# Optimization experiments

Measured on AMD Instinct MI355X. Metric: run time of the kernel, lower is better.

Reference implementation:

```python
import math
import jax, jax.numpy as jnp
import numpy as np

N_HEADS = 16
NUM_BUCKETS = 32
MAX_DISTANCE = 128
ROTARY_BASE = 10000.0


def rotate_half(x):
    x1, x2 = jnp.split(x, 2, axis=-1)
    return jnp.concatenate((-x2, x1), axis=-1)


def rotary_freqs(T, dim):
    inv_freq = 1.0 / (ROTARY_BASE ** (jnp.arange(0, dim, 2, dtype=jnp.float32) / dim))
    t = jnp.arange(T, dtype=jnp.float32)
    freqs = jnp.einsum('i,j->ij', t, inv_freq)  # [T, dim/2]
    return jnp.concatenate((freqs, freqs), axis=-1)  # [T, dim]


def rel_pos_bucket_causal(rel_pos, num_buckets=NUM_BUCKETS, max_distance=MAX_DISTANCE):
    n = jnp.maximum(-rel_pos, 0)  # [T, T] int
    max_exact = num_buckets // 2
    is_small = n < max_exact
    n_safe = jnp.maximum(n, 1).astype(jnp.float32)
    val_if_large = max_exact + (
        jnp.log(n_safe / max_exact) / math.log(max_distance / max_exact) * (num_buckets - max_exact)
    ).astype(jnp.int32)
    val_if_large = jnp.minimum(val_if_large, num_buckets - 1)
    return jnp.where(is_small, n, val_if_large)


def setup_inputs() -> dict:
    key = jax.random.key(0)
    ks = jax.random.split(key, 10)
    B, T, C = 2, 2048, 1024
    s = 0.02
    return {
        'x':  jax.random.normal(ks[0], (B, T, C), dtype=jnp.float32),
        'Wq': jax.random.normal(ks[1], (C, C), dtype=jnp.float32) * s,
        'bq': jnp.zeros((C,), dtype=jnp.float32),
        'Wk': jax.random.normal(ks[2], (C, C), dtype=jnp.float32) * s,
        'bk': jnp.zeros((C,), dtype=jnp.float32),
        'Wv': jax.random.normal(ks[3], (C, C), dtype=jnp.float32) * s,
        'bv': jnp.zeros((C,), dtype=jnp.float32),
        'Wp': jax.random.normal(ks[4], (C, C), dtype=jnp.float32) * s,
        'bp': jnp.zeros((C,), dtype=jnp.float32),
        'rel_bias_table': jax.random.normal(ks[5], (NUM_BUCKETS, N_HEADS), dtype=jnp.float32) * s,
    }


def reference(x, Wq, bq, Wk, bk, Wv, bv, Wp, bp, rel_bias_table):
    B, T, C = x.shape
    H = N_HEADS
    D = C // H

    def heads(y):
        return y.reshape(B, T, H, D).transpose(0, 2, 1, 3)  # [B,H,T,D]

    q = heads(x @ Wq + bq)
    k = heads(x @ Wk + bk)
    v = heads(x @ Wv + bv)

    # rotary (use_xpos=False -> scale=1)
    freqs = rotary_freqs(T, D)  # [T, D]
    cos, sin = jnp.cos(freqs), jnp.sin(freqs)
    q = q * cos + rotate_half(q) * sin
    k = k * cos + rotate_half(k) * sin

    # relative position bias (causal, scale=1.0)
    pos = jnp.arange(T)
    rel_pos = pos[None, :] - pos[:, None]  # k_pos - q_pos
    bucket = rel_pos_bucket_causal(rel_pos)  # [T, T]
    bias = rel_bias_table[bucket]  # [T, T, H]
    bias = bias.transpose(2, 0, 1)  # [H, T, T]

    att = jnp.einsum('bhid,bhjd->bhij', q, k) + bias[None]
    att = att * (1.0 / math.sqrt(D))
    causal = pos[None, :] <= pos[:, None]  # tril mask [T, T]
    att = jnp.where(causal[None, None], att, -jnp.inf)
    att = jax.nn.softmax(att, axis=-1)

    y = jnp.einsum('bhij,bhjd->bhid', att, v)  # [B,H,T,D]
    y = y.transpose(0, 2, 1, 3).reshape(B, T, C)
    return y @ Wp + bp
```

## Files before the change

kernel.cpp:

```cpp
#include <hip/hip_runtime.h>
#include <hip/hip_bf16.h>
#include <math.h>

#define B_ 2
#define T_ 2048
#define C_ 1024
#define H_ 16
#define D_ 64
#define M_ (B_ * T_)
#define K_ 1024

#define SCALE2 0.18033688011112043f

typedef short bf16x8 __attribute__((ext_vector_type(8)));
typedef float f32x4  __attribute__((ext_vector_type(4)));
typedef unsigned int u32;

__device__ __forceinline__ float u2f(unsigned short u) {
    union { unsigned int i; float f; } v; v.i = ((unsigned int)u) << 16; return v.f;
}
__device__ __forceinline__ unsigned short f2b(float f) {
    __hip_bfloat16 h = __float2bfloat16(f);
    return *reinterpret_cast<unsigned short*>(&h);
}
__device__ __forceinline__ u32 pack_bf16_rnd(float a, float b) {
    const u32 au = __float_as_uint(a) + 0x8000u;
    const u32 bu = __float_as_uint(b) + 0x8000u;
    return __builtin_amdgcn_perm(bu, au, 0x07060302u);
}
__device__ __forceinline__ void load_lds16(const void* g, void* l) {
    __builtin_amdgcn_global_load_lds(
        (const __attribute__((address_space(1))) u32*)g,
        (__attribute__((address_space(3))) u32*)l, 16, 0, 0);
}

__global__ __launch_bounds__(256) void prep(
    const float* __restrict__ x,
    const float* __restrict__ W0, const float* __restrict__ W1,
    const float* __restrict__ W2, const float* __restrict__ W3,
    const float* __restrict__ tbl,
    unsigned short* __restrict__ xb,
    unsigned short* __restrict__ T0, unsigned short* __restrict__ T1,
    unsigned short* __restrict__ T2, unsigned short* __restrict__ T3,
    float* __restrict__ dtab, float2* __restrict__ trig)
{
    __shared__ __align__(16) unsigned short tile[64][72];
    const int bx = blockIdx.x;
    const int tid = threadIdx.x;

    if (bx < 2048) {
        const int idx = bx * 256 + tid;
        const float4 a = reinterpret_cast<const float4*>(x)[idx * 2];
        const float4 b = reinterpret_cast<const float4*>(x)[idx * 2 + 1];
        unsigned short t[8] = {f2b(a.x), f2b(a.y), f2b(a.z), f2b(a.w),
                               f2b(b.x), f2b(b.y), f2b(b.z), f2b(b.w)};
        reinterpret_cast<bf16x8*>(xb)[idx] = *reinterpret_cast<const bf16x8*>(t);
    } else if (bx < 3072) {
        const int w = bx - 2048;
        const int z = w >> 8;
        const int rem = w & 255;
        const int k0 = (rem & 15) * 64, n0 = (rem >> 4) * 64;
        const float* W = z == 0 ? W0 : z == 1 ? W1 : z == 2 ? W2 : W3;
        unsigned short* Wt = z == 0 ? T0 : z == 1 ? T1 : z == 2 ? T2 : T3;

        #pragma unroll
        for (int it = 0; it < 4; ++it) {
            const int idx = it * 256 + tid;
            const int r = idx >> 4, c = (idx & 15) * 4;
            const float4 w4 = *reinterpret_cast<const float4*>(W + (size_t)(k0 + r) * C_ + n0 + c);
            tile[r][c + 0] = f2b(w4.x); tile[r][c + 1] = f2b(w4.y);
            tile[r][c + 2] = f2b(w4.z); tile[r][c + 3] = f2b(w4.w);
        }
        __syncthreads();
        #pragma unroll
        for (int it = 0; it < 2; ++it) {
            const int idx = it * 256 + tid;
            const int nc = idx >> 3, kc = (idx & 7) * 8;
            unsigned short tmp[8];
            #pragma unroll
            for (int e = 0; e < 8; ++e) tmp[e] = tile[kc + e][nc];
            *reinterpret_cast<bf16x8*>(Wt + (size_t)(n0 + nc) * K_ + k0 + kc) =
                *reinterpret_cast<const bf16x8*>(tmp);
        }
    } else {
        const int idx = (bx - 3072) * 256 + tid;
        if (idx < H_ * T_) {
            const int h = idx >> 11, n = idx & (T_ - 1);
            int bucket;
            if (n < 16) bucket = n;
            else {
                int vb = 16 + (int)(log2f((float)n * 0.0625f) * (16.0f / 3.0f));
                bucket = vb < 31 ? vb : 31;
            }
            dtab[idx] = tbl[bucket * H_ + h] * SCALE2;
        }
        const int t = idx >> 5, j = idx & 31;
        const float inv = exp2f(-(float)j * (13.287712379549449f / 32.0f));
        const float ang = (float)t * inv;
        trig[idx] = make_float2(cosf(ang), sinf(ang));
    }
}

template<int BN>
__device__ __forceinline__ void gemm_core(
    const unsigned short* __restrict__ A, const unsigned short* __restrict__ Bt,
    const float* __restrict__ bias, const float2* __restrict__ trig,
    float rot_scale, float* __restrict__ outf,
    unsigned short* __restrict__ outb, int mode, int m0, int n0)
{
    constexpr int FN  = BN / 32;
    constexpr int BCH = BN / 64;
    constexpr int NLD = 2 + BCH;
    __shared__ __align__(16) unsigned short As0[128 * 32];
    __shared__ __align__(16) unsigned short As1[128 * 32];
    __shared__ __align__(16) unsigned short As2[128 * 32];
    __shared__ __align__(16) unsigned short Bs0[BN * 32];
    __shared__ __align__(16) unsigned short Bs1[BN * 32];
    __shared__ __align__(16) unsigned short Bs2[BN * 32];

    const int tid = threadIdx.x;
    const int wid = tid >> 6, lane = tid & 63;
    const int l16 = lane & 15, quad = lane >> 4;
    const int wm = wid >> 1, wn = wid & 1;

    f32x4 acc[4][FN];
    #pragma unroll
    for (int i = 0; i < 4; ++i)
        #pragma unroll
        for (int j = 0; j < FN; ++j) acc[i][j] = (f32x4){0.f, 0.f, 0.f, 0.f};

    auto stage = [&](unsigned short* Asb, unsigned short* Bsb, int k0) {
        #pragma unroll
        for (int it = 0; it < 2; ++it) {
            const int idx = it * 256 + tid;
            const int row = idx >> 2, ch = (idx & 3) * 8;
            load_lds16(A + (size_t)(m0 + row) * K_ + k0 + ch,
                       (char*)Asb + it * 4096 + wid * 1024);
        }
        #pragma unroll
        for (int it = 0; it < BCH; ++it) {
            const int idx = it * 256 + tid;
            const int row = idx >> 2, ch = (idx & 3) * 8;
            load_lds16(Bt + (size_t)(n0 + row) * K_ + k0 + ch,
                       (char*)Bsb + it * 4096 + wid * 1024);
        }
    };
    auto compute = [&](const unsigned short* Asb, const unsigned short* Bsb) {
        bf16x8 af[4], bf[FN];
        #pragma unroll
        for (int i = 0; i < 4; ++i)
            af[i] = *reinterpret_cast<const bf16x8*>(&Asb[(wm * 64 + i * 16 + l16) * 32 + quad * 8]);
        #pragma unroll
        for (int j = 0; j < FN; ++j)
            bf[j] = *reinterpret_cast<const bf16x8*>(&Bsb[(wn * (BN / 2) + j * 16 + l16) * 32 + quad * 8]);
        #pragma unroll
        for (int i = 0; i < 4; ++i)
            #pragma unroll
            for (int j = 0; j < FN; ++j)
                acc[i][j] = __builtin_amdgcn_mfma_f32_16x16x32_bf16(af[i], bf[j], acc[i][j], 0, 0, 0);
    };
    auto step = [&](const unsigned short* cA, const unsigned short* cB,
                    unsigned short* nA, unsigned short* nB, int kn, bool do_stage) {
        if constexpr (NLD == 4) asm volatile("s_waitcnt vmcnt(4)" ::: "memory");
        else                    asm volatile("s_waitcnt vmcnt(3)" ::: "memory");
        __builtin_amdgcn_s_barrier();
        __builtin_amdgcn_sched_barrier(0);
        if (do_stage) stage(nA, nB, kn);
        compute(cA, cB);
    };

    stage(As0, Bs0, 0);
    stage(As1, Bs1, 32);

    for (int kb = 0; kb < 30; kb += 3) {
        step(As0, Bs0, As2, Bs2, (kb + 2) * 32, true);
        step(As1, Bs1, As0, Bs0, (kb + 3) * 32, true);
        step(As2, Bs2, As1, Bs1, (kb + 4) * 32, true);
    }
    step(As0, Bs0, As2, Bs2, 0, false);
    asm volatile("s_waitcnt vmcnt(0)" ::: "memory");
    __builtin_amdgcn_s_barrier();
    __builtin_amdgcn_sched_barrier(0);
    compute(As1, Bs1);

    if (mode == 1) {
        #pragma unroll
        for (int i = 0; i < 4; ++i) {
            const int mb = m0 + wm * 64 + i * 16 + quad * 4;
            const int bb = mb >> 11, tb = mb & (T_ - 1);
            #pragma unroll
            for (int jc = 0; jc < FN / 2; ++jc) {
                const int n_lo = n0 + wn * (BN / 2) + jc * 16 + l16;
                const int h = n_lo >> 6, d = n_lo & 63;
                const float bv_lo = bias[n_lo], bv_hi = bias[n_lo + 32];
                unsigned short* po = outb + (((size_t)bb * H_ + h) * T_ + tb) * D_ + d;
                #pragma unroll
                for (int r = 0; r < 4; ++r) {
                    const float2 cs = trig[(tb + r) * 32 + d];
                    const float a = acc[i][jc][r] + bv_lo;
                    const float b = acc[i][jc + FN / 2][r] + bv_hi;
                    po[(size_t)r * D_]      = f2b((a * cs.x - b * cs.y) * rot_scale);
                    po[(size_t)r * D_ + 32] = f2b((b * cs.x + a * cs.y) * rot_scale);
                }
            }
        }
        return;
    }

    #pragma unroll
    for (int i = 0; i < 4; ++i) {
        const int mb = m0 + wm * 64 + i * 16 + quad * 4;
        #pragma unroll
        for (int j = 0; j < FN; ++j) {
            const int n = n0 + wn * (BN / 2) + j * 16 + l16;
            const float bv = bias[n];
            if (mode == 2) {
                const int bb = mb >> 11, t = mb & (T_ - 1);
                const int h = n >> 6, d = n & 63;
                uint2 w;
                w.x = pack_bf16_rnd(acc[i][j][0] + bv, acc[i][j][1] + bv);
                w.y = pack_bf16_rnd(acc[i][j][2] + bv, acc[i][j][3] + bv);
                *reinterpret_cast<uint2*>(
                    outb + (((size_t)bb * H_ + h) * D_ + d) * T_ + t) = w;
            } else {
                #pragma unroll
                for (int r = 0; r < 4; ++r)
                    outf[(size_t)(mb + r) * C_ + n] = acc[i][j][r] + bv;
            }
        }
    }
}

__global__ __launch_bounds__(256) void gemm_qkv(
    const unsigned short* __restrict__ A,
    const unsigned short* __restrict__ Wq, const unsigned short* __restrict__ Wk,
    const unsigned short* __restrict__ Wv,
    const float* __restrict__ bq, const float* __restrict__ bk,
    const float* __restrict__ bv, const float2* __restrict__ trig,
    unsigned short* __restrict__ Qo, unsigned short* __restrict__ Ko,
    unsigned short* __restrict__ Vto)
{
    const int lin = (int)blockIdx.x;
    const int g = lin & 7, slot = lin >> 3;
    const int w = g * 96 + slot;
    const int z = w >> 8, rem = w & 255;
    const int m0 = (rem >> 3) * 128, n0 = (rem & 7) * 128;

    const unsigned short* Bt = z == 0 ? Wq : z == 1 ? Wk : Wv;
    const float* bias = z == 0 ? bq : z == 1 ? bk : bv;
    unsigned short* outb = z == 0 ? Qo : z == 1 ? Ko : Vto;
    const float rs = z == 0 ? SCALE2 : 1.0f;
    gemm_core<128>(A, Bt, bias, trig, rs, nullptr, outb, z == 2 ? 2 : 1, m0, n0);
}

__global__ __launch_bounds__(256) void gemm_proj(
    const unsigned short* __restrict__ A, const unsigned short* __restrict__ Bt,
    const float* __restrict__ bias, float* __restrict__ outf)
{
    const int lin = (int)blockIdx.x;
    const int g = lin & 7, slot = lin >> 3;
    const int w = g * 32 + slot;
    const int m0 = (w >> 3) * 128, n0 = (w & 7) * 128;
    gemm_core<128>(A, Bt, bias, nullptr, 1.0f, outf, nullptr, 0, m0, n0);
}

__device__ __forceinline__ int kv_swz(int row, int col8) {
    return row * 64 + ((col8 ^ ((row ^ (row >> 2)) & 7)) * 8);
}

__global__ __launch_bounds__(256) void flash_attn(
    const unsigned short* __restrict__ Q, const unsigned short* __restrict__ K,
    const unsigned short* __restrict__ Vt, const float* __restrict__ dtab,
    unsigned short* __restrict__ Y)
{
    __shared__ __align__(16) unsigned short Ks[2][64 * 64];
    __shared__ __align__(16) unsigned short Vs[2][64 * 64];
    __shared__ __align__(16) unsigned short Ps[4][16][72];
    __shared__ __align__(16) float bias_ls[64 + T_];

    const int lin = (int)(blockIdx.y * gridDim.x + blockIdx.x);
    const int bh  = lin & 31;
    const int rem = lin >> 5;
    const int h = bh & (H_ - 1), b = bh >> 4;
    const int tid = threadIdx.x;
    const int wid = tid >> 6, lane = tid & 63;
    const int l16 = lane & 15, quad = lane >> 4;
    const size_t base = (size_t)bh * T_ * D_;
    const size_t vbase = (size_t)bh * D_ * T_;

    const int qta = (rem + bh) & 15;
    const int qtb = 31 - qta;

    if (tid < 64) bias_ls[tid] = -INFINITY;
    for (int ii = tid; ii < qtb * 64 + 64; ii += 256) bias_ls[64 + ii] = dtab[h * T_ + ii];

    bf16x8 ones;
    #pragma unroll
    for (int e = 0; e < 8; ++e) ones[e] = (short)0x3F80;

    const int sr0 = tid >> 3,         sc80 = tid & 7;
    const int sr1 = (tid + 256) >> 3, sc81 = (tid + 256) & 7;
    const int wo0 = kv_swz(sr0, sc80), wo1 = kv_swz(sr1, sc81);
    const int sch0 = sc80 * 8, sch1 = sc81 * 8;

    int kro[4][2], vro[4][2];
    #pragma unroll
    for (int c = 0; c < 4; ++c)
        #pragma unroll
        for (int s = 0; s < 2; ++s) {
            kro[c][s] = kv_swz(l16 * 4 + c, s * 4 + quad);
            vro[c][s] = kv_swz(c * 16 + l16, s * 4 + quad);
        }

    bf16x8 kr[2], vr[2];
    kr[0] = *reinterpret_cast<const bf16x8*>(K + base + (size_t)sr0 * D_ + sch0);
    kr[1] = *reinterpret_cast<const bf16x8*>(K + base + (size_t)sr1 * D_ + sch1);
    vr[0] = *reinterpret_cast<const bf16x8*>(Vt + vbase + (size_t)sr0 * T_ + sch0);
    vr[1] = *reinterpret_cast<const bf16x8*>(Vt + vbase + (size_t)sr1 * T_ + sch1);
    *reinterpret_cast<bf16x8*>(&Ks[0][wo0]) = kr[0];
    *reinterpret_cast<bf16x8*>(&Ks[0][wo1]) = kr[1];
    *reinterpret_cast<bf16x8*>(&Vs[0][wo0]) = vr[0];
    *reinterpret_cast<bf16x8*>(&Vs[0][wo1]) = vr[1];
    kr[0] = *reinterpret_cast<const bf16x8*>(K + base + (size_t)(64 + sr0) * D_ + sch0);
    kr[1] = *reinterpret_cast<const bf16x8*>(K + base + (size_t)(64 + sr1) * D_ + sch1);
    vr[0] = *reinterpret_cast<const bf16x8*>(Vt + vbase + (size_t)sr0 * T_ + 64 + sch0);
    vr[1] = *reinterpret_cast<const bf16x8*>(Vt + vbase + (size_t)sr1 * T_ + 64 + sch1);
    __syncthreads();

    int t = 0;
    for (int qi = 0; qi < 2; ++qi) {
        const int qt = qi ? qta : qtb;
        const int q0 = qt * 64;
        const int arow = q0 + wid * 16 + l16;
        const int crow = q0 + wid * 16 + quad * 4;
        const int nbase = crow - l16 * 4;

        bf16x8 qf[2];
        qf[0] = *reinterpret_cast<const bf16x8*>(Q + base + (size_t)arow * D_ + quad * 8);
        qf[1] = *reinterpret_cast<const bf16x8*>(Q + base + (size_t)arow * D_ + 32 + quad * 8);

        f32x4 o[4], ol;
        #pragma unroll
        for (int c = 0; c < 4; ++c) o[c] = (f32x4){0.f, 0.f, 0.f, 0.f};
        ol = (f32x4){0.f, 0.f, 0.f, 0.f};

        for (int kt = 0; kt <= qt; ++kt, ++t) {
            const int j0 = kt * 64;
            const int cur = t & 1, nxt = cur ^ 1;

            if (t < 32) {
                *reinterpret_cast<bf16x8*>(&Ks[nxt][wo0]) = kr[0];
                *reinterpret_cast<bf16x8*>(&Ks[nxt][wo1]) = kr[1];
                *reinterpret_cast<bf16x8*>(&Vs[nxt][wo0]) = vr[0];
                *reinterpret_cast<bf16x8*>(&Vs[nxt][wo1]) = vr[1];
            }
            if (t < 31) {
                const int tn = t + 2;
                const int jn = (tn <= qtb ? tn : tn - qtb - 1) * 64;
                kr[0] = *reinterpret_cast<const bf16x8*>(K + base + (size_t)(jn + sr0) * D_ + sch0);
                kr[1] = *reinterpret_cast<const bf16x8*>(K + base + (size_t)(jn + sr1) * D_ + sch1);
                vr[0] = *reinterpret_cast<const bf16x8*>(Vt + vbase + (size_t)sr0 * T_ + jn + sch0);
                vr[1] = *reinterpret_cast<const bf16x8*>(Vt + vbase + (size_t)sr1 * T_ + jn + sch1);
            }

            const int d0 = nbase - j0;
            const f32x4 blo = *reinterpret_cast<const f32x4*>(&bias_ls[60 + d0]);
            const f32x4 bhi = *reinterpret_cast<const f32x4*>(&bias_ls[64 + d0]);

            f32x4 sc[4];
            #pragma unroll
            for (int c = 0; c < 4; ++c) {
                #pragma unroll
                for (int r = 0; r < 4; ++r)
                    sc[c][r] = (r >= c) ? bhi[r - c] : blo[4 + r - c];
            }
            __builtin_amdgcn_s_setprio(1);
            #pragma unroll
            for (int c = 0; c < 4; ++c) {
                #pragma unroll
                for (int s = 0; s < 2; ++s) {
                    bf16x8 kf = *reinterpret_cast<const bf16x8*>(&Ks[cur][kro[c][s]]);
                    sc[c] = __builtin_amdgcn_mfma_f32_16x16x32_bf16(qf[s], kf, sc[c], 0, 0, 0);
                }
            }
            __builtin_amdgcn_s_setprio(0);

            #pragma unroll
            for (int r = 0; r < 4; ++r) {
                const float p0 = __builtin_amdgcn_exp2f(sc[0][r]);
                const float p1 = __builtin_amdgcn_exp2f(sc[1][r]);
                const float p2 = __builtin_amdgcn_exp2f(sc[2][r]);
                const float p3 = __builtin_amdgcn_exp2f(sc[3][r]);
                uint2 w;
                w.x = pack_bf16_rnd(p0, p1);
                w.y = pack_bf16_rnd(p2, p3);
                *reinterpret_cast<uint2*>(&Ps[wid][quad * 4 + r][l16 * 4]) = w;
            }

            __builtin_amdgcn_s_setprio(1);
            #pragma unroll
            for (int s = 0; s < 2; ++s) {
                bf16x8 pf = *reinterpret_cast<const bf16x8*>(&Ps[wid][l16][s * 32 + quad * 8]);
                #pragma unroll
                for (int c = 0; c < 4; ++c) {
                    bf16x8 vf = *reinterpret_cast<const bf16x8*>(&Vs[cur][vro[c][s]]);
                    o[c] = __builtin_amdgcn_mfma_f32_16x16x32_bf16(pf, vf, o[c], 0, 0, 0);
                }
                ol = __builtin_amdgcn_mfma_f32_16x16x32_bf16(pf, ones, ol, 0, 0, 0);
            }
            __builtin_amdgcn_s_setprio(0);

            __syncthreads();
        }

        #pragma unroll
        for (int r = 0; r < 4; ++r) {
            const int i = crow + r;
            const float invl = 1.0f / ol[r];
            #pragma unroll
            for (int c = 0; c < 4; ++c)
                Y[((size_t)b * T_ + i) * C_ + h * D_ + c * 16 + l16] = f2b(o[c][r] * invl);
        }
    }
}

extern "C" void kernel_launch(void* const* d_in, const int* in_sizes, int n_in,
                              void* d_out, int out_size, void* d_ws, size_t ws_size,
                              hipStream_t stream)
{
    const float* x   = (const float*)d_in[0];
    const float* Wq  = (const float*)d_in[1];
    const float* bq  = (const float*)d_in[2];
    const float* Wk  = (const float*)d_in[3];
    const float* bk  = (const float*)d_in[4];
    const float* Wv  = (const float*)d_in[5];
    const float* bv  = (const float*)d_in[6];
    const float* Wp  = (const float*)d_in[7];
    const float* bp  = (const float*)d_in[8];
    const float* tbl = (const float*)d_in[9];
    float* out = (float*)d_out;

    const size_t n1 = (size_t)B_ * H_ * T_ * D_;
    const size_t nW = (size_t)C_ * C_;
    unsigned short* xb  = (unsigned short*)d_ws;
    unsigned short* Wqt = xb + (size_t)M_ * K_;
    unsigned short* Wkt = Wqt + nW;
    unsigned short* Wvt = Wkt + nW;
    unsigned short* Wpt = Wvt + nW;
    unsigned short* Qb  = Wpt + nW;
    unsigned short* Kb  = Qb + n1;
    unsigned short* Vtb = Kb + n1;
    unsigned short* Yb  = Vtb + n1;
    float* dtab = (float*)(Yb + n1);
    float2* trig = (float2*)(dtab + H_ * T_);

    const dim3 blk(256);

    prep<<<dim3(3328), blk, 0, stream>>>(x, Wq, Wk, Wv, Wp, tbl,
                                         xb, Wqt, Wkt, Wvt, Wpt, dtab, trig);

    gemm_qkv<<<dim3(768), blk, 0, stream>>>(
        xb, Wqt, Wkt, Wvt, bq, bk, bv, trig, Qb, Kb, Vtb);

    flash_attn<<<dim3(16, B_ * H_), blk, 0, stream>>>(Qb, Kb, Vtb, dtab, Yb);

    gemm_proj<<<dim3(256), blk, 0, stream>>>(Yb, Wpt, bp, out);
}
```

Before: 191.3 us.

## Fuse all stages into one cooperative persistent kernel with grid syncs

Merges prep, QKV GEMM, flash attention and output projection into a single cooperative kernel of 768 blocks, separated by grid-wide syncs, with all LDS buffers shared and aliased across stages. The aim is to remove three kernel launch gaps and their tail effects. The P tile in attention now goes through an XOR-swizzled LDS layout to cut bank conflicts. If the cooperative launch fails, the code falls back to the separate kernels. The trade-offs are that only 512 or 256 of the 768 blocks are busy in the later stages, and occupancy is capped at 3 blocks per CU.

```diff
diff --git a/kernel.cpp b/kernel.cpp
--- a/kernel.cpp
+++ b/kernel.cpp
@@ -1,6 +1,9 @@
 #include <hip/hip_runtime.h>
+#include <hip/hip_cooperative_groups.h>
 #include <hip/hip_bf16.h>
 #include <math.h>
+
+namespace cg = cooperative_groups;
 
 #define B_ 2
 #define T_ 2048
@@ -16,9 +19,10 @@
 typedef float f32x4  __attribute__((ext_vector_type(4)));
 typedef unsigned int u32;
 
-__device__ __forceinline__ float u2f(unsigned short u) {
-    union { unsigned int i; float f; } v; v.i = ((unsigned int)u) << 16; return v.f;
-}
+#define AS0_SZ (128 * 32 + 64)
+#define BUF_SZ (128 * 32)
+#define BS2_SZ (128 * 32 + 128)
+
 __device__ __forceinline__ unsigned short f2b(float f) {
     __hip_bfloat16 h = __float2bfloat16(f);
     return *reinterpret_cast<unsigned short*>(&h);
@@ -33,8 +37,12 @@
         (const __attribute__((address_space(1))) u32*)g,
         (__attribute__((address_space(3))) u32*)l, 16, 0, 0);
 }
-
-__global__ __launch_bounds__(256) void prep(
+__device__ __forceinline__ int kv_swz(int row, int col8) {
+    return row * 64 + ((col8 ^ ((row ^ (row >> 2)) & 7)) * 8);
+}
+
+__device__ __forceinline__ void prep_unit(
+    int u, int tid, unsigned short (*tile)[65],
     const float* __restrict__ x,
     const float* __restrict__ W0, const float* __restrict__ W1,
     const float* __restrict__ W2, const float* __restrict__ W3,
@@ -44,19 +52,15 @@
     unsigned short* __restrict__ T2, unsigned short* __restrict__ T3,
     float* __restrict__ dtab, float2* __restrict__ trig)
 {
-    __shared__ __align__(16) unsigned short tile[64][72];
-    const int bx = blockIdx.x;
-    const int tid = threadIdx.x;
-
-    if (bx < 2048) {
-        const int idx = bx * 256 + tid;
+    if (u < 2048) {
+        const int idx = u * 256 + tid;
         const float4 a = reinterpret_cast<const float4*>(x)[idx * 2];
         const float4 b = reinterpret_cast<const float4*>(x)[idx * 2 + 1];
         unsigned short t[8] = {f2b(a.x), f2b(a.y), f2b(a.z), f2b(a.w),
                                f2b(b.x), f2b(b.y), f2b(b.z), f2b(b.w)};
         reinterpret_cast<bf16x8*>(xb)[idx] = *reinterpret_cast<const bf16x8*>(t);
-    } else if (bx < 3072) {
-        const int w = bx - 2048;
+    } else if (u < 3072) {
+        const int w = u - 2048;
         const int z = w >> 8;
         const int rem = w & 255;
         const int k0 = (rem & 15) * 64, n0 = (rem >> 4) * 64;
@@ -82,8 +86,9 @@
             *reinterpret_cast<bf16x8*>(Wt + (size_t)(n0 + nc) * K_ + k0 + kc) =
                 *reinterpret_cast<const bf16x8*>(tmp);
         }
+        __syncthreads();
     } else {
-        const int idx = (bx - 3072) * 256 + tid;
+        const int idx = (u - 3072) * 256 + tid;
         if (idx < H_ * T_) {
             const int h = idx >> 11, n = idx & (T_ - 1);
             int bucket;
@@ -101,33 +106,25 @@
     }
 }
 
-template<int BN>
-__device__ __forceinline__ void gemm_core(
+__device__ __forceinline__ void gemm_core128(
+    unsigned short* __restrict__ As0, unsigned short* __restrict__ As1,
+    unsigned short* __restrict__ As2, unsigned short* __restrict__ Bs0,
+    unsigned short* __restrict__ Bs1, unsigned short* __restrict__ Bs2,
     const unsigned short* __restrict__ A, const unsigned short* __restrict__ Bt,
     const float* __restrict__ bias, const float2* __restrict__ trig,
     float rot_scale, float* __restrict__ outf,
     unsigned short* __restrict__ outb, int mode, int m0, int n0)
 {
-    constexpr int FN  = BN / 32;
-    constexpr int BCH = BN / 64;
-    constexpr int NLD = 2 + BCH;
-    __shared__ __align__(16) unsigned short As0[128 * 32];
-    __shared__ __align__(16) unsigned short As1[128 * 32];
-    __shared__ __align__(16) unsigned short As2[128 * 32];
-    __shared__ __align__(16) unsigned short Bs0[BN * 32];
-    __shared__ __align__(16) unsigned short Bs1[BN * 32];
-    __shared__ __align__(16) unsigned short Bs2[BN * 32];
-
     const int tid = threadIdx.x;
     const int wid = tid >> 6, lane = tid & 63;
     const int l16 = lane & 15, quad = lane >> 4;
     const int wm = wid >> 1, wn = wid & 1;
 
-    f32x4 acc[4][FN];
+    f32x4 acc[4][4];
     #pragma unroll
     for (int i = 0; i < 4; ++i)
         #pragma unroll
-        for (int j = 0; j < FN; ++j) acc[i][j] = (f32x4){0.f, 0.f, 0.f, 0.f};
+        for (int j = 0; j < 4; ++j) acc[i][j] = (f32x4){0.f, 0.f, 0.f, 0.f};
 
     auto stage = [&](unsigned short* Asb, unsigned short* Bsb, int k0) {
         #pragma unroll
@@ -136,33 +133,26 @@
             const int row = idx >> 2, ch = (idx & 3) * 8;
             load_lds16(A + (size_t)(m0 + row) * K_ + k0 + ch,
                        (char*)Asb + it * 4096 + wid * 1024);
-        }
-        #pragma unroll
-        for (int it = 0; it < BCH; ++it) {
-            const int idx = it * 256 + tid;
-            const int row = idx >> 2, ch = (idx & 3) * 8;
             load_lds16(Bt + (size_t)(n0 + row) * K_ + k0 + ch,
                        (char*)Bsb + it * 4096 + wid * 1024);
         }
     };
     auto compute = [&](const unsigned short* Asb, const unsigned short* Bsb) {
-        bf16x8 af[4], bf[FN];
+        bf16x8 af[4], bf[4];
+        #pragma unroll
+        for (int i = 0; i < 4; ++i) {
+            af[i] = *reinterpret_cast<const bf16x8*>(&Asb[(wm * 64 + i * 16 + l16) * 32 + quad * 8]);
+            bf[i] = *reinterpret_cast<const bf16x8*>(&Bsb[(wn * 64 + i * 16 + l16) * 32 + quad * 8]);
+        }
         #pragma unroll
         for (int i = 0; i < 4; ++i)
-            af[i] = *reinterpret_cast<const bf16x8*>(&Asb[(wm * 64 + i * 16 + l16) * 32 + quad * 8]);
-        #pragma unroll
-        for (int j = 0; j < FN; ++j)
-            bf[j] = *reinterpret_cast<const bf16x8*>(&Bsb[(wn * (BN / 2) + j * 16 + l16) * 32 + quad * 8]);
-        #pragma unroll
-        for (int i = 0; i < 4; ++i)
-            #pragma unroll
-            for (int j = 0; j < FN; ++j)
+            #pragma unroll
+            for (int j = 0; j < 4; ++j)
                 acc[i][j] = __builtin_amdgcn_mfma_f32_16x16x32_bf16(af[i], bf[j], acc[i][j], 0, 0, 0);
     };
     auto step = [&](const unsigned short* cA, const unsigned short* cB,
                     unsigned short* nA, unsigned short* nB, int kn, bool do_stage) {
-        if constexpr (NLD == 4) asm volatile("s_waitcnt vmcnt(4)" ::: "memory");
-        else                    asm volatile("s_waitcnt vmcnt(3)" ::: "memory");
+        asm volatile("s_waitcnt vmcnt(4)" ::: "memory");
         __builtin_amdgcn_s_barrier();
         __builtin_amdgcn_sched_barrier(0);
         if (do_stage) stage(nA, nB, kn);
@@ -189,8 +179,8 @@
             const int mb = m0 + wm * 64 + i * 16 + quad * 4;
             const int bb = mb >> 11, tb = mb & (T_ - 1);
             #pragma unroll
-            for (int jc = 0; jc < FN / 2; ++jc) {
-                const int n_lo = n0 + wn * (BN / 2) + jc * 16 + l16;
+            for (int jc = 0; jc < 2; ++jc) {
+                const int n_lo = n0 + wn * 64 + jc * 16 + l16;
                 const int h = n_lo >> 6, d = n_lo & 63;
                 const float bv_lo = bias[n_lo], bv_hi = bias[n_lo + 32];
                 unsigned short* po = outb + (((size_t)bb * H_ + h) * T_ + tb) * D_ + d;
@@ -198,7 +188,7 @@
                 for (int r = 0; r < 4; ++r) {
                     const float2 cs = trig[(tb + r) * 32 + d];
                     const float a = acc[i][jc][r] + bv_lo;
-                    const float b = acc[i][jc + FN / 2][r] + bv_hi;
+                    const float b = acc[i][jc + 2][r] + bv_hi;
                     po[(size_t)r * D_]      = f2b((a * cs.x - b * cs.y) * rot_scale);
                     po[(size_t)r * D_ + 32] = f2b((b * cs.x + a * cs.y) * rot_scale);
                 }
@@ -211,8 +201,8 @@
     for (int i = 0; i < 4; ++i) {
         const int mb = m0 + wm * 64 + i * 16 + quad * 4;
         #pragma unroll
-        for (int j = 0; j < FN; ++j) {
-            const int n = n0 + wn * (BN / 2) + j * 16 + l16;
+        for (int j = 0; j < 4; ++j) {
+            const int n = n0 + wn * 64 + j * 16 + l16;
             const float bv = bias[n];
             if (mode == 2) {
                 const int bb = mb >> 11, t = mb & (T_ - 1);
@@ -231,54 +221,17 @@
     }
 }
 
-__global__ __launch_bounds__(256) void gemm_qkv(
-    const unsigned short* __restrict__ A,
-    const unsigned short* __restrict__ Wq, const unsigned short* __restrict__ Wk,
-    const unsigned short* __restrict__ Wv,
-    const float* __restrict__ bq, const float* __restrict__ bk,
-    const float* __restrict__ bv, const float2* __restrict__ trig,
-    unsigned short* __restrict__ Qo, unsigned short* __restrict__ Ko,
-    unsigned short* __restrict__ Vto)
-{
-    const int lin = (int)blockIdx.x;
-    const int g = lin & 7, slot = lin >> 3;
-    const int w = g * 96 + slot;
-    const int z = w >> 8, rem = w & 255;
-    const int m0 = (rem >> 3) * 128, n0 = (rem & 7) * 128;
-
-    const unsigned short* Bt = z == 0 ? Wq : z == 1 ? Wk : Wv;
-    const float* bias = z == 0 ? bq : z == 1 ? bk : bv;
-    unsigned short* outb = z == 0 ? Qo : z == 1 ? Ko : Vto;
-    const float rs = z == 0 ? SCALE2 : 1.0f;
-    gemm_core<128>(A, Bt, bias, trig, rs, nullptr, outb, z == 2 ? 2 : 1, m0, n0);
-}
-
-__global__ __launch_bounds__(256) void gemm_proj(
-    const unsigned short* __restrict__ A, const unsigned short* __restrict__ Bt,
-    const float* __restrict__ bias, float* __restrict__ outf)
-{
-    const int lin = (int)blockIdx.x;
-    const int g = lin & 7, slot = lin >> 3;
-    const int w = g * 32 + slot;
-    const int m0 = (w >> 3) * 128, n0 = (w & 7) * 128;
-    gemm_core<128>(A, Bt, bias, nullptr, 1.0f, outf, nullptr, 0, m0, n0);
-}
-
-__device__ __forceinline__ int kv_swz(int row, int col8) {
-    return row * 64 + ((col8 ^ ((row ^ (row >> 2)) & 7)) * 8);
-}
-
-__global__ __launch_bounds__(256) void flash_attn(
+__device__ __forceinline__ void flash_body(
+    int lin,
+    unsigned short* __restrict__ As0, unsigned short* __restrict__ As1,
+    unsigned short* __restrict__ As2, unsigned short* __restrict__ Bs0,
+    unsigned short* __restrict__ Bs1, unsigned short* __restrict__ Bs2,
     const unsigned short* __restrict__ Q, const unsigned short* __restrict__ K,
     const unsigned short* __restrict__ Vt, const float* __restrict__ dtab,
     unsigned short* __restrict__ Y)
 {
-    __shared__ __align__(16) unsigned short Ks[2][64 * 64];
-    __shared__ __align__(16) unsigned short Vs[2][64 * 64];
-    __shared__ __align__(16) unsigned short Ps[4][16][72];
-    __shared__ __align__(16) float bias_ls[64 + T_];
-
-    const int lin = (int)(blockIdx.y * gridDim.x + blockIdx.x);
+    float* bias_ls = reinterpret_cast<float*>(Bs2);
+
     const int bh  = lin & 31;
     const int rem = lin >> 5;
     const int h = bh & (H_ - 1), b = bh >> 4;
@@ -312,15 +265,26 @@
             vro[c][s] = kv_swz(c * 16 + l16, s * 4 + quad);
         }
 
+    unsigned short* PsW = Bs1 + wid * 1024;
+    int pwo[4], pro[2];
+    #pragma unroll
+    for (int r = 0; r < 4; ++r) {
+        const int row = quad * 4 + r;
+        pwo[r] = row * 64 + (((l16 >> 1) ^ (row & 7)) << 3) + ((l16 & 1) << 2);
+    }
+    #pragma unroll
+    for (int s = 0; s < 2; ++s)
+        pro[s] = l16 * 64 + (((s * 4 + quad) ^ (l16 & 7)) << 3);
+
     bf16x8 kr[2], vr[2];
     kr[0] = *reinterpret_cast<const bf16x8*>(K + base + (size_t)sr0 * D_ + sch0);
     kr[1] = *reinterpret_cast<const bf16x8*>(K + base + (size_t)sr1 * D_ + sch1);
     vr[0] = *reinterpret_cast<const bf16x8*>(Vt + vbase + (size_t)sr0 * T_ + sch0);
     vr[1] = *reinterpret_cast<const bf16x8*>(Vt + vbase + (size_t)sr1 * T_ + sch1);
-    *reinterpret_cast<bf16x8*>(&Ks[0][wo0]) = kr[0];
-    *reinterpret_cast<bf16x8*>(&Ks[0][wo1]) = kr[1];
-    *reinterpret_cast<bf16x8*>(&Vs[0][wo0]) = vr[0];
-    *reinterpret_cast<bf16x8*>(&Vs[0][wo1]) = vr[1];
+    *reinterpret_cast<bf16x8*>(&As0[wo0]) = kr[0];
+    *reinterpret_cast<bf16x8*>(&As0[wo1]) = kr[1];
+    *reinterpret_cast<bf16x8*>(&As2[wo0]) = vr[0];
+    *reinterpret_cast<bf16x8*>(&As2[wo1]) = vr[1];
     kr[0] = *reinterpret_cast<const bf16x8*>(K + base + (size_t)(64 + sr0) * D_ + sch0);
     kr[1] = *reinterpret_cast<const bf16x8*>(K + base + (size_t)(64 + sr1) * D_ + sch1);
     vr[0] = *reinterpret_cast<const bf16x8*>(Vt + vbase + (size_t)sr0 * T_ + 64 + sch0);
@@ -346,13 +310,17 @@
 
         for (int kt = 0; kt <= qt; ++kt, ++t) {
             const int j0 = kt * 64;
-            const int cur = t & 1, nxt = cur ^ 1;
+            const int cur = t & 1;
+            const unsigned short* Kc = cur ? As1 : As0;
+            unsigned short*       Kn = cur ? As0 : As1;
+            const unsigned short* Vc = cur ? Bs0 : As2;
+            unsigned short*       Vn = cur ? As2 : Bs0;
 
             if (t < 32) {
-                *reinterpret_cast<bf16x8*>(&Ks[nxt][wo0]) = kr[0];
-                *reinterpret_cast<bf16x8*>(&Ks[nxt][wo1]) = kr[1];
-                *reinterpret_cast<bf16x8*>(&Vs[nxt][wo0]) = vr[0];
-                *reinterpret_cast<bf16x8*>(&Vs[nxt][wo1]) = vr[1];
+                *reinterpret_cast<bf16x8*>(&Kn[wo0]) = kr[0];
+                *reinterpret_cast<bf16x8*>(&Kn[wo1]) = kr[1];
+                *reinterpret_cast<bf16x8*>(&Vn[wo0]) = vr[0];
+                *reinterpret_cast<bf16x8*>(&Vn[wo1]) = vr[1];
             }
             if (t < 31) {
                 const int tn = t + 2;
@@ -379,7 +347,7 @@
             for (int c = 0; c < 4; ++c) {
                 #pragma unroll
                 for (int s = 0; s < 2; ++s) {
-                    bf16x8 kf = *reinterpret_cast<const bf16x8*>(&Ks[cur][kro[c][s]]);
+                    bf16x8 kf = *reinterpret_cast<const bf16x8*>(&Kc[kro[c][s]]);
                     sc[c] = __builtin_amdgcn_mfma_f32_16x16x32_bf16(qf[s], kf, sc[c], 0, 0, 0);
                 }
             }
@@ -394,16 +362,16 @@
                 uint2 w;
                 w.x = pack_bf16_rnd(p0, p1);
                 w.y = pack_bf16_rnd(p2, p3);
-                *reinterpret_cast<uint2*>(&Ps[wid][quad * 4 + r][l16 * 4]) = w;
+                *reinterpret_cast<uint2*>(PsW + pwo[r]) = w;
             }
 
             __builtin_amdgcn_s_setprio(1);
             #pragma unroll
             for (int s = 0; s < 2; ++s) {
-                bf16x8 pf = *reinterpret_cast<const bf16x8*>(&Ps[wid][l16][s * 32 + quad * 8]);
+                bf16x8 pf = *reinterpret_cast<const bf16x8*>(PsW + pro[s]);
                 #pragma unroll
                 for (int c = 0; c < 4; ++c) {
-                    bf16x8 vf = *reinterpret_cast<const bf16x8*>(&Vs[cur][vro[c][s]]);
+                    bf16x8 vf = *reinterpret_cast<const bf16x8*>(&Vc[vro[c][s]]);
                     o[c] = __builtin_amdgcn_mfma_f32_16x16x32_bf16(pf, vf, o[c], 0, 0, 0);
                 }
                 ol = __builtin_amdgcn_mfma_f32_16x16x32_bf16(pf, ones, ol, 0, 0, 0);
@@ -422,6 +390,134 @@
                 Y[((size_t)b * T_ + i) * C_ + h * D_ + c * 16 + l16] = f2b(o[c][r] * invl);
         }
     }
+}
+
+__global__ __launch_bounds__(256, 3) void fused(
+    const float* x, const float* Wq, const float* bq, const float* Wk,
+    const float* bk, const float* Wv, const float* bv, const float* Wp,
+    const float* bp, const float* tbl,
+    unsigned short* xb, unsigned short* Wqt, unsigned short* Wkt,
+    unsigned short* Wvt, unsigned short* Wpt,
+    unsigned short* Qb, unsigned short* Kb, unsigned short* Vtb,
+    unsigned short* Yb, float* dtab, float2* trig, float* out)
+{
+    __shared__ __align__(16) unsigned short As0[AS0_SZ];
+    __shared__ __align__(16) unsigned short As1[BUF_SZ];
+    __shared__ __align__(16) unsigned short As2[BUF_SZ];
+    __shared__ __align__(16) unsigned short Bs0[BUF_SZ];
+    __shared__ __align__(16) unsigned short Bs1[BUF_SZ];
+    __shared__ __align__(16) unsigned short Bs2[BS2_SZ];
+
+    const int bid = (int)blockIdx.x;
+    const int tid = (int)threadIdx.x;
+    cg::grid_group grid = cg::this_grid();
+
+    for (int u = bid; u < 3328; u += 768)
+        prep_unit(u, tid, reinterpret_cast<unsigned short(*)[65]>(As0),
+                  x, Wq, Wk, Wv, Wp, tbl, xb, Wqt, Wkt, Wvt, Wpt, dtab, trig);
+    grid.sync();
+
+    {
+        const int g = bid & 7, slot = bid >> 3;
+        const int w = g * 96 + slot;
+        const int z = w >> 8, rem = w & 255;
+        const int m0 = (rem >> 3) * 128, n0 = (rem & 7) * 128;
+        const unsigned short* Bt = z == 0 ? Wqt : z == 1 ? Wkt : Wvt;
+        const float* bias = z == 0 ? bq : z == 1 ? bk : bv;
+        unsigned short* outb = z == 0 ? Qb : z == 1 ? Kb : Vtb;
+        const float rs = z == 0 ? SCALE2 : 1.0f;
+        gemm_core128(As0, As1, As2, Bs0, Bs1, Bs2,
+                     xb, Bt, bias, trig, rs, nullptr, outb, z == 2 ? 2 : 1, m0, n0);
+    }
+    grid.sync();
+
+    if (bid < 512)
+        flash_body(bid, As0, As1, As2, Bs0, Bs1, Bs2, Qb, Kb, Vtb, dtab, Yb);
+    grid.sync();
+
+    if (bid < 256) {
+        const int g = bid & 7, slot = bid >> 3;
+        const int w = g * 32 + slot;
+        const int m0 = (w >> 3) * 128, n0 = (w & 7) * 128;
+        gemm_core128(As0, As1, As2, Bs0, Bs1, Bs2,
+                     Yb, Wpt, bp, nullptr, 1.0f, out, nullptr, 0, m0, n0);
+    }
+}
+
+__global__ __launch_bounds__(256) void prep_k(
+    const float* __restrict__ x,
+    const float* __restrict__ W0, const float* __restrict__ W1,
+    const float* __restrict__ W2, const float* __restrict__ W3,
+    const float* __restrict__ tbl,
+    unsigned short* __restrict__ xb,
+    unsigned short* __restrict__ T0, unsigned short* __restrict__ T1,
+    unsigned short* __restrict__ T2, unsigned short* __restrict__ T3,
+    float* __restrict__ dtab, float2* __restrict__ trig)
+{
+    __shared__ __align__(16) unsigned short tile[64][65];
+    prep_unit((int)blockIdx.x, (int)threadIdx.x, tile,
+              x, W0, W1, W2, W3, tbl, xb, T0, T1, T2, T3, dtab, trig);
+}
+
+__global__ __launch_bounds__(256) void gemm_qkv_k(
+    const unsigned short* __restrict__ A,
+    const unsigned short* __restrict__ Wq, const unsigned short* __restrict__ Wk,
+    const unsigned short* __restrict__ Wv,
+    const float* __restrict__ bq, const float* __restrict__ bk,
+    const float* __restrict__ bv, const float2* __restrict__ trig,
+    unsigned short* __restrict__ Qo, unsigned short* __restrict__ Ko,
+    unsigned short* __restrict__ Vto)
+{
+    __shared__ __align__(16) unsigned short As0[BUF_SZ];
+    __shared__ __align__(16) unsigned short As1[BUF_SZ];
+    __shared__ __align__(16) unsigned short As2[BUF_SZ];
+    __shared__ __align__(16) unsigned short Bs0[BUF_SZ];
+    __shared__ __align__(16) unsigned short Bs1[BUF_SZ];
+    __shared__ __align__(16) unsigned short Bs2[BUF_SZ];
+    const int lin = (int)blockIdx.x;
+    const int g = lin & 7, slot = lin >> 3;
+    const int w = g * 96 + slot;
+    const int z = w >> 8, rem = w & 255;
+    const int m0 = (rem >> 3) * 128, n0 = (rem & 7) * 128;
+    const unsigned short* Bt = z == 0 ? Wq : z == 1 ? Wk : Wv;
+    const float* bias = z == 0 ? bq : z == 1 ? bk : bv;
+    unsigned short* outb = z == 0 ? Qo : z == 1 ? Ko : Vto;
+    const float rs = z == 0 ? SCALE2 : 1.0f;
+    gemm_core128(As0, As1, As2, Bs0, Bs1, Bs2,
+                 A, Bt, bias, trig, rs, nullptr, outb, z == 2 ? 2 : 1, m0, n0);
+}
+
+__global__ __launch_bounds__(256) void gemm_proj_k(
+    const unsigned short* __restrict__ A, const unsigned short* __restrict__ Bt,
+    const float* __restrict__ bias, float* __restrict__ outf)
+{
+    __shared__ __align__(16) unsigned short As0[BUF_SZ];
+    __shared__ __align__(16) unsigned short As1[BUF_SZ];
+    __shared__ __align__(16) unsigned short As2[BUF_SZ];
+    __shared__ __align__(16) unsigned short Bs0[BUF_SZ];
+    __shared__ __align__(16) unsigned short Bs1[BUF_SZ];
+    __shared__ __align__(16) unsigned short Bs2[BUF_SZ];
+    const int lin = (int)blockIdx.x;
+    const int g = lin & 7, slot = lin >> 3;
+    const int w = g * 32 + slot;
+    const int m0 = (w >> 3) * 128, n0 = (w & 7) * 128;
+    gemm_core128(As0, As1, As2, Bs0, Bs1, Bs2,
+                 A, Bt, bias, nullptr, 1.0f, outf, nullptr, 0, m0, n0);
+}
+
+__global__ __launch_bounds__(256) void flash_attn_k(
+    const unsigned short* __restrict__ Q, const unsigned short* __restrict__ K,
+    const unsigned short* __restrict__ Vt, const float* __restrict__ dtab,
+    unsigned short* __restrict__ Y)
+{
+    __shared__ __align__(16) unsigned short As0[BUF_SZ];
+    __shared__ __align__(16) unsigned short As1[BUF_SZ];
+    __shared__ __align__(16) unsigned short As2[BUF_SZ];
+    __shared__ __align__(16) unsigned short Bs0[BUF_SZ];
+    __shared__ __align__(16) unsigned short Bs1[BUF_SZ];
+    __shared__ __align__(16) unsigned short Bs2[BS2_SZ];
+    const int lin = (int)(blockIdx.y * gridDim.x + blockIdx.x);
+    flash_body(lin, As0, As1, As2, Bs0, Bs1, Bs2, Q, K, Vt, dtab, Y);
 }
 
 extern "C" void kernel_launch(void* const* d_in, const int* in_sizes, int n_in,
@@ -454,15 +550,24 @@
     float* dtab = (float*)(Yb + n1);
     float2* trig = (float2*)(dtab + H_ * T_);
 
-    const dim3 blk(256);
-
-    prep<<<dim3(3328), blk, 0, stream>>>(x, Wq, Wk, Wv, Wp, tbl,
-                                         xb, Wqt, Wkt, Wvt, Wpt, dtab, trig);
-
-    gemm_qkv<<<dim3(768), blk, 0, stream>>>(
-        xb, Wqt, Wkt, Wvt, bq, bk, bv, trig, Qb, Kb, Vtb);
-
-    flash_attn<<<dim3(16, B_ * H_), blk, 0, stream>>>(Qb, Kb, Vtb, dtab, Yb);
-
-    gemm_proj<<<dim3(256), blk, 0, stream>>>(Yb, Wpt, bp, out);
-}
+    void* args[] = {
+        (void*)&x, (void*)&Wq, (void*)&bq, (void*)&Wk, (void*)&bk,
+        (void*)&Wv, (void*)&bv, (void*)&Wp, (void*)&bp, (void*)&tbl,
+        (void*)&xb, (void*)&Wqt, (void*)&Wkt, (void*)&Wvt, (void*)&Wpt,
+        (void*)&Qb, (void*)&Kb, (void*)&Vtb, (void*)&Yb,
+        (void*)&dtab, (void*)&trig, (void*)&out };
+
+    hipError_t e = hipLaunchCooperativeKernel(
+        (const void*)fused, dim3(768), dim3(256), args, 0, stream);
+
+    if (e != hipSuccess) {
+        (void)hipGetLastError();
+        const dim3 blk(256);
+        prep_k<<<dim3(3328), blk, 0, stream>>>(x, Wq, Wk, Wv, Wp, tbl,
+                                               xb, Wqt, Wkt, Wvt, Wpt, dtab, trig);
+        gemm_qkv_k<<<dim3(768), blk, 0, stream>>>(
+            xb, Wqt, Wkt, Wvt, bq, bk, bv, trig, Qb, Kb, Vtb);
+        flash_attn_k<<<dim3(16, B_ * H_), blk, 0, stream>>>(Qb, Kb, Vtb, dtab, Yb);
+        gemm_proj_k<<<dim3(256), blk, 0, stream>>>(Yb, Wpt, bp, out);
+    }
+}
```

Result: slower. 482.1 us (+152.0%).

## Split paired causal query tiles into one block per tile, longest first

Applied to the files above, without the earlier changes.

The attention kernel previously gave each block two complementary query tiles (qt and 31-qt) to balance causal work. It now launches 1024 blocks with one query tile each, ordered so the longest tiles are dispatched first, and relies on the hardware scheduler to balance the load. It also adds a minimum-occupancy hint of three blocks per CU and replaces the end-of-iteration __syncthreads with an explicit LDS wait, barrier and scheduling fence that are skipped on the last iteration. The risk is more per-block setup (bias table and first K/V tile loads) and a tail of short blocks, in exchange for finer-grained scheduling and possibly higher occupancy.

```diff
diff --git a/kernel.cpp b/kernel.cpp
--- a/kernel.cpp
+++ b/kernel.cpp
@@ -16,9 +16,6 @@
 typedef float f32x4  __attribute__((ext_vector_type(4)));
 typedef unsigned int u32;
 
-__device__ __forceinline__ float u2f(unsigned short u) {
-    union { unsigned int i; float f; } v; v.i = ((unsigned int)u) << 16; return v.f;
-}
 __device__ __forceinline__ unsigned short f2b(float f) {
     __hip_bfloat16 h = __float2bfloat16(f);
     return *reinterpret_cast<unsigned short*>(&h);
@@ -268,7 +265,7 @@
     return row * 64 + ((col8 ^ ((row ^ (row >> 2)) & 7)) * 8);
 }
 
-__global__ __launch_bounds__(256) void flash_attn(
+__global__ __launch_bounds__(256, 3) void flash_attn(
     const unsigned short* __restrict__ Q, const unsigned short* __restrict__ K,
     const unsigned short* __restrict__ Vt, const float* __restrict__ dtab,
     unsigned short* __restrict__ Y)
@@ -278,21 +275,19 @@
     __shared__ __align__(16) unsigned short Ps[4][16][72];
     __shared__ __align__(16) float bias_ls[64 + T_];
 
-    const int lin = (int)(blockIdx.y * gridDim.x + blockIdx.x);
+    const int lin = (int)blockIdx.x;
     const int bh  = lin & 31;
-    const int rem = lin >> 5;
+    const int qt  = 31 - (lin >> 5);
     const int h = bh & (H_ - 1), b = bh >> 4;
     const int tid = threadIdx.x;
     const int wid = tid >> 6, lane = tid & 63;
     const int l16 = lane & 15, quad = lane >> 4;
     const size_t base = (size_t)bh * T_ * D_;
     const size_t vbase = (size_t)bh * D_ * T_;
-
-    const int qta = (rem + bh) & 15;
-    const int qtb = 31 - qta;
+    const int q0 = qt * 64;
 
     if (tid < 64) bias_ls[tid] = -INFINITY;
-    for (int ii = tid; ii < qtb * 64 + 64; ii += 256) bias_ls[64 + ii] = dtab[h * T_ + ii];
+    for (int ii = tid; ii < q0 + 64; ii += 256) bias_ls[64 + ii] = dtab[h * T_ + ii];
 
     bf16x8 ones;
     #pragma unroll
@@ -327,100 +322,98 @@
     vr[1] = *reinterpret_cast<const bf16x8*>(Vt + vbase + (size_t)sr1 * T_ + 64 + sch1);
     __syncthreads();
 
-    int t = 0;
-    for (int qi = 0; qi < 2; ++qi) {
-        const int qt = qi ? qta : qtb;
-        const int q0 = qt * 64;
-        const int arow = q0 + wid * 16 + l16;
-        const int crow = q0 + wid * 16 + quad * 4;
-        const int nbase = crow - l16 * 4;
-
-        bf16x8 qf[2];
-        qf[0] = *reinterpret_cast<const bf16x8*>(Q + base + (size_t)arow * D_ + quad * 8);
-        qf[1] = *reinterpret_cast<const bf16x8*>(Q + base + (size_t)arow * D_ + 32 + quad * 8);
-
-        f32x4 o[4], ol;
-        #pragma unroll
-        for (int c = 0; c < 4; ++c) o[c] = (f32x4){0.f, 0.f, 0.f, 0.f};
-        ol = (f32x4){0.f, 0.f, 0.f, 0.f};
-
-        for (int kt = 0; kt <= qt; ++kt, ++t) {
-            const int j0 = kt * 64;
-            const int cur = t & 1, nxt = cur ^ 1;
-
-            if (t < 32) {
-                *reinterpret_cast<bf16x8*>(&Ks[nxt][wo0]) = kr[0];
-                *reinterpret_cast<bf16x8*>(&Ks[nxt][wo1]) = kr[1];
-                *reinterpret_cast<bf16x8*>(&Vs[nxt][wo0]) = vr[0];
-                *reinterpret_cast<bf16x8*>(&Vs[nxt][wo1]) = vr[1];
+    const int arow = q0 + wid * 16 + l16;
+    const int crow = q0 + wid * 16 + quad * 4;
+    const int nbase = crow - l16 * 4;
+
+    bf16x8 qf[2];
+    qf[0] = *reinterpret_cast<const bf16x8*>(Q + base + (size_t)arow * D_ + quad * 8);
+    qf[1] = *reinterpret_cast<const bf16x8*>(Q + base + (size_t)arow * D_ + 32 + quad * 8);
+
+    f32x4 o[4], ol;
+    #pragma unroll
+    for (int c = 0; c < 4; ++c) o[c] = (f32x4){0.f, 0.f, 0.f, 0.f};
+    ol = (f32x4){0.f, 0.f, 0.f, 0.f};
+
+    for (int kt = 0; kt <= qt; ++kt) {
+        const int j0 = kt * 64;
+        const int cur = kt & 1, nxt = cur ^ 1;
+
+        if (kt < qt) {
+            *reinterpret_cast<bf16x8*>(&Ks[nxt][wo0]) = kr[0];
+            *reinterpret_cast<bf16x8*>(&Ks[nxt][wo1]) = kr[1];
+            *reinterpret_cast<bf16x8*>(&Vs[nxt][wo0]) = vr[0];
+            *reinterpret_cast<bf16x8*>(&Vs[nxt][wo1]) = vr[1];
+        }
+        if (kt < qt - 1) {
+            const int jn = j0 + 128;
+            kr[0] = *reinterpret_cast<const bf16x8*>(K + base + (size_t)(jn + sr0) * D_ + sch0);
+            kr[1] = *reinterpret_cast<const bf16x8*>(K + base + (size_t)(jn + sr1) * D_ + sch1);
+            vr[0] = *reinterpret_cast<const bf16x8*>(Vt + vbase + (size_t)sr0 * T_ + jn + sch0);
+            vr[1] = *reinterpret_cast<const bf16x8*>(Vt + vbase + (size_t)sr1 * T_ + jn + sch1);
+        }
+
+        const int d0 = nbase - j0;
+        const f32x4 blo = *reinterpret_cast<const f32x4*>(&bias_ls[60 + d0]);
+        const f32x4 bhi = *reinterpret_cast<const f32x4*>(&bias_ls[64 + d0]);
+
+        f32x4 sc[4];
+        #pragma unroll
+        for (int c = 0; c < 4; ++c) {
+            #pragma unroll
+            for (int r = 0; r < 4; ++r)
+                sc[c][r] = (r >= c) ? bhi[r - c] : blo[4 + r - c];
+        }
+        __builtin_amdgcn_s_setprio(1);
+        #pragma unroll
+        for (int c = 0; c < 4; ++c) {
+            #pragma unroll
+            for (int s = 0; s < 2; ++s) {
+                bf16x8 kf = *reinterpret_cast<const bf16x8*>(&Ks[cur][kro[c][s]]);
+                sc[c] = __builtin_amdgcn_mfma_f32_16x16x32_bf16(qf[s], kf, sc[c], 0, 0, 0);
             }
-            if (t < 31) {
-                const int tn = t + 2;
-                const int jn = (tn <= qtb ? tn : tn - qtb - 1) * 64;
-                kr[0] = *reinterpret_cast<const bf16x8*>(K + base + (size_t)(jn + sr0) * D_ + sch0);
-                kr[1] = *reinterpret_cast<const bf16x8*>(K + base + (size_t)(jn + sr1) * D_ + sch1);
-                vr[0] = *reinterpret_cast<const bf16x8*>(Vt + vbase + (size_t)sr0 * T_ + jn + sch0);
-                vr[1] = *reinterpret_cast<const bf16x8*>(Vt + vbase + (size_t)sr1 * T_ + jn + sch1);
+        }
+        __builtin_amdgcn_s_setprio(0);
+
+        #pragma unroll
+        for (int r = 0; r < 4; ++r) {
+            const float p0 = __builtin_amdgcn_exp2f(sc[0][r]);
+            const float p1 = __builtin_amdgcn_exp2f(sc[1][r]);
+            const float p2 = __builtin_amdgcn_exp2f(sc[2][r]);
+            const float p3 = __builtin_amdgcn_exp2f(sc[3][r]);
+            uint2 w;
+            w.x = pack_bf16_rnd(p0, p1);
+            w.y = pack_bf16_rnd(p2, p3);
+            *reinterpret_cast<uint2*>(&Ps[wid][quad * 4 + r][l16 * 4]) = w;
+        }
+
+        __builtin_amdgcn_s_setprio(1);
+        #pragma unroll
+        for (int s = 0; s < 2; ++s) {
+            bf16x8 pf = *reinterpret_cast<const bf16x8*>(&Ps[wid][l16][s * 32 + quad * 8]);
+            #pragma unroll
+            for (int c = 0; c < 4; ++c) {
+                bf16x8 vf = *reinterpret_cast<const bf16x8*>(&Vs[cur][vro[c][s]]);
+                o[c] = __builtin_amdgcn_mfma_f32_16x16x32_bf16(pf, vf, o[c], 0, 0, 0);
             }
-
-            const int d0 = nbase - j0;
-            const f32x4 blo = *reinterpret_cast<const f32x4*>(&bias_ls[60 + d0]);
-            const f32x4 bhi = *reinterpret_cast<const f32x4*>(&bias_ls[64 + d0]);
-
-            f32x4 sc[4];
-            #pragma unroll
-            for (int c = 0; c < 4; ++c) {
-                #pragma unroll
-                for (int r = 0; r < 4; ++r)
-                    sc[c][r] = (r >= c) ? bhi[r - c] : blo[4 + r - c];
-            }
-            __builtin_amdgcn_s_setprio(1);
-            #pragma unroll
-            for (int c = 0; c < 4; ++c) {
-                #pragma unroll
-                for (int s = 0; s < 2; ++s) {
-                    bf16x8 kf = *reinterpret_cast<const bf16x8*>(&Ks[cur][kro[c][s]]);
-                    sc[c] = __builtin_amdgcn_mfma_f32_16x16x32_bf16(qf[s], kf, sc[c], 0, 0, 0);
-                }
-            }
-            __builtin_amdgcn_s_setprio(0);
-
-            #pragma unroll
-            for (int r = 0; r < 4; ++r) {
-                const float p0 = __builtin_amdgcn_exp2f(sc[0][r]);
-                const float p1 = __builtin_amdgcn_exp2f(sc[1][r]);
-                const float p2 = __builtin_amdgcn_exp2f(sc[2][r]);
-                const float p3 = __builtin_amdgcn_exp2f(sc[3][r]);
-                uint2 w;
-                w.x = pack_bf16_rnd(p0, p1);
-                w.y = pack_bf16_rnd(p2, p3);
-                *reinterpret_cast<uint2*>(&Ps[wid][quad * 4 + r][l16 * 4]) = w;
-            }
-
-            __builtin_amdgcn_s_setprio(1);
-            #pragma unroll
-            for (int s = 0; s < 2; ++s) {
-                bf16x8 pf = *reinterpret_cast<const bf16x8*>(&Ps[wid][l16][s * 32 + quad * 8]);
-                #pragma unroll
-                for (int c = 0; c < 4; ++c) {
-                    bf16x8 vf = *reinterpret_cast<const bf16x8*>(&Vs[cur][vro[c][s]]);
-                    o[c] = __builtin_amdgcn_mfma_f32_16x16x32_bf16(pf, vf, o[c], 0, 0, 0);
-                }
-                ol = __builtin_amdgcn_mfma_f32_16x16x32_bf16(pf, ones, ol, 0, 0, 0);
-            }
-            __builtin_amdgcn_s_setprio(0);
-
-            __syncthreads();
-        }
-
-        #pragma unroll
-        for (int r = 0; r < 4; ++r) {
-            const int i = crow + r;
-            const float invl = 1.0f / ol[r];
-            #pragma unroll
-            for (int c = 0; c < 4; ++c)
-                Y[((size_t)b * T_ + i) * C_ + h * D_ + c * 16 + l16] = f2b(o[c][r] * invl);
-        }
+            ol = __builtin_amdgcn_mfma_f32_16x16x32_bf16(pf, ones, ol, 0, 0, 0);
+        }
+        __builtin_amdgcn_s_setprio(0);
+
+        if (kt < qt) {
+            asm volatile("s_waitcnt lgkmcnt(0)" ::: "memory");
+            __builtin_amdgcn_s_barrier();
+            __builtin_amdgcn_sched_barrier(0);
+        }
+    }
+
+    #pragma unroll
+    for (int r = 0; r < 4; ++r) {
+        const int i = crow + r;
+        const float invl = 1.0f / ol[r];
+        #pragma unroll
+        for (int c = 0; c < 4; ++c)
+            Y[((size_t)b * T_ + i) * C_ + h * D_ + c * 16 + l16] = f2b(o[c][r] * invl);
     }
 }
 
@@ -462,7 +455,7 @@
     gemm_qkv<<<dim3(768), blk, 0, stream>>>(
         xb, Wqt, Wkt, Wvt, bq, bk, bv, trig, Qb, Kb, Vtb);
 
-    flash_attn<<<dim3(16, B_ * H_), blk, 0, stream>>>(Qb, Kb, Vtb, dtab, Yb);
+    flash_attn<<<dim3(1024), blk, 0, stream>>>(Qb, Kb, Vtb, dtab, Yb);
 
     gemm_proj<<<dim3(256), blk, 0, stream>>>(Yb, Wpt, bp, out);
 }
```

Result: no change. 188.3 us (-1.6%).
